# Optimization experiments

Hardware: AMD Instinct MI355X
Metric: run time of the kernel (lower is better)

Reference implementation:

```python
import jax, jax.numpy as jnp
import numpy as np

B, N, M, E, H = 8, 256, 512, 1024, 32
D = E // H
SCALING = D ** -0.5
BIG_DIST = 1e6


def setup_inputs() -> dict:
    key = jax.random.key(0)
    ks = jax.random.split(key, 12)
    w = lambda k: jax.random.normal(k, (E, E), jnp.float32) * 0.02
    return {
        "x": jax.random.normal(ks[0], (N, B, E), jnp.float32),
        "pos": jax.random.normal(ks[1], (B, N, 3), jnp.float32) * 3.0,
        "expand_pos": jax.random.normal(ks[2], (B, M, 3), jnp.float32) * 3.0,
        "attn_bias": jax.random.normal(ks[3], (B, H, N, N + M), jnp.float32) * 0.1,
        "padding_mask": jnp.zeros((B, N), bool),
        "expand_mask": jnp.zeros((B, M), bool),
        "outcell_index": jax.random.randint(ks[4], (B, M), 0, N),
        "Wq": w(ks[5]), "Wk": w(ks[6]), "Wv": w(ks[7]),
        "Wve": w(ks[8]), "Wo": w(ks[9]), "Woe": w(ks[10]),
    }


def reference(x, pos, expand_pos, attn_bias, padding_mask, expand_mask,
              outcell_index, Wq, Wk, Wv, Wve, Wo, Woe):
    xb = jnp.swapaxes(x, 0, 1)              # [B, N, E]
    b, n, e = xb.shape

    all_pos = jnp.concatenate([pos, expand_pos], axis=1)   # [B, EXT, 3]
    delta = pos[:, :, None, :] - all_pos[:, None, :, :]     # [B, N, EXT, 3]
    full_mask = jnp.concatenate([padding_mask, expand_mask], axis=-1)  # [B, EXT]

    dist = jnp.linalg.norm(delta, axis=-1)                  # [B, N, EXT]
    dist = jnp.where(padding_mask[:, :, None], BIG_DIST, dist)
    dist = jnp.where(full_mask[:, None, :], BIG_DIST, dist)
    delta = delta / (dist[..., None] + 1.0)

    q = (xb @ Wq.T) * SCALING
    k = xb @ Wk.T
    v = xb @ Wv.T
    ve = xb @ Wve.T

    gather = lambda t: jnp.take_along_axis(t, outcell_index[..., None], axis=1)
    k = jnp.concatenate([k, gather(k)], axis=1)             # [B, EXT, E]
    v = jnp.concatenate([v, gather(v)], axis=1)
    ve = jnp.concatenate([ve, gather(ve)], axis=1)
    ext = k.shape[1]

    qh = q.reshape(b, n, H, D).transpose(0, 2, 1, 3)        # [B, H, N, D]
    kh = k.reshape(b, ext, H, D).transpose(0, 2, 1, 3)
    vh = v.reshape(b, ext, H, D).transpose(0, 2, 1, 3)
    veh = ve.reshape(b, ext, H, D).transpose(0, 2, 1, 3)

    attn = jnp.einsum('bhnd,bhmd->bhnm', qh, kh) + attn_bias
    neg = jnp.finfo(jnp.float32).min
    attn = jnp.where(full_mask[:, None, None, :], neg, attn)
    attn = jnp.where(padding_mask[:, None, :, None], neg, attn)
    probs = jax.nn.softmax(attn.astype(jnp.float32), axis=-1).astype(attn.dtype)

    delta = jnp.where(padding_mask[:, :, None, None], 0.0, delta)

    # equivariant vector output: (probs ⊗ delta) contracted with v
    vec = jnp.einsum('bhnm,bnmc,bhmd->bnchd', probs, delta, vh)  # [B,N,3,H,D]
    vec_out = vec.reshape(b, n, 3, e) @ Wo.T

    xo = jnp.einsum('bhnm,bhmd->bnhd', probs, veh).reshape(b, n, e) @ Woe.T
    return (xo, vec_out)
```

## Files before the change

### kernel.cpp

```cpp
#include <hip/hip_runtime.h>


typedef unsigned short u16;
typedef unsigned int u32;
typedef short short8 __attribute__((ext_vector_type(8)));
typedef float float4v __attribute__((ext_vector_type(4)));

#define SCALING 0.17677669529663687f
#define LOG2E 1.4426950408889634f

__device__ __forceinline__ u16 f2b(float f) {
  union { float f; u32 u; } v; v.f = f;
  return (u16)((v.u + 0x7FFFu + ((v.u >> 16) & 1u)) >> 16);
}
__device__ __forceinline__ float b2f(short s) {
  union { u32 u; float f; } v; v.u = ((u32)(u16)s) << 16;
  return v.f;
}
__device__ __forceinline__ float4v mfma16(short8 a, short8 b, float4v c) {
  return __builtin_amdgcn_mfma_f32_16x16x32_bf16(a, b, c, 0, 0, 0);
}
__device__ __forceinline__ void gll16(const void* g, void* l) {
  __builtin_amdgcn_global_load_lds((const __attribute__((address_space(1))) void*)g,
                                   (__attribute__((address_space(3))) void*)l, 16, 0, 0);
}

__global__ __launch_bounds__(256) void convert_kernel(
    const float* __restrict__ x, const float* __restrict__ Wq,
    const float* __restrict__ Wk, const float* __restrict__ Wv,
    const float* __restrict__ Wve, const float* __restrict__ Wo,
    const float* __restrict__ Woe, u16* __restrict__ xb,
    u16* __restrict__ Wcat, u16* __restrict__ Woe_b, u16* __restrict__ Wo_b) {
  const int idx = blockIdx.x * 256 + threadIdx.x;
  const int stride = gridDim.x * 256;
  for (int i = idx; i < 2048 * 1024; i += stride) {
    const int row = i >> 10, e = i & 1023;
    const int b = row >> 8, n = row & 255;
    xb[i] = f2b(x[((size_t)n * 8 + b) * 1024 + e]);
  }
  for (int i = idx; i < 1024 * 1024; i += stride) {
    Wcat[i] = f2b(Wq[i]);
    Wcat[1048576 + i] = f2b(Wk[i]);
    Wcat[2097152 + i] = f2b(Wv[i]);
    Wcat[3145728 + i] = f2b(Wve[i]);
    Woe_b[i] = f2b(Woe[i]);
    Wo_b[i] = f2b(Wo[i]);
  }
}

__global__ __launch_bounds__(256) void gemm_bt(
    const u16* __restrict__ A, const u16* __restrict__ W_lo,
    const u16* __restrict__ W_hi, int split_row, float* __restrict__ C,
    int Ndim, int Kdim) {
  __shared__ __align__(16) u16 sA[128 * 32];
  __shared__ __align__(16) u16 sB[128 * 32];
  const int tid = threadIdx.x, wave = tid >> 6, lane = tid & 63;
  const int quad = lane >> 4, l15 = lane & 15;
  const int row0 = blockIdx.y * 128, col0 = blockIdx.x * 128;
  const u16* W = (row0 < split_row) ? W_lo : W_hi;
  const int wr = (wave >> 1) * 64, wc = (wave & 1) * 64;
  const int sr = lane >> 2, sc = lane & 3;
  float4v acc[4][4] = {};
  const u16* gA = A + (size_t)row0 * Kdim;
  const u16* gW = W + (size_t)col0 * Kdim;
  for (int k0 = 0; k0 < Kdim; k0 += 32) {
    __syncthreads();
#pragma unroll
    for (int i = 0; i < 2; ++i) {
      const int r = wave * 32 + i * 16 + sr;
      gll16(gA + (size_t)r * Kdim + k0 + sc * 8, (char*)sA + (wave * 32 + i * 16) * 64);
      gll16(gW + (size_t)r * Kdim + k0 + sc * 8, (char*)sB + (wave * 32 + i * 16) * 64);
    }
    __syncthreads();
    short8 af[4], bf[4];
#pragma unroll
    for (int t = 0; t < 4; ++t) {
      af[t] = *(const short8*)(sA + (wr + t * 16 + l15) * 32 + quad * 8);
      bf[t] = *(const short8*)(sB + (wc + t * 16 + l15) * 32 + quad * 8);
    }
#pragma unroll
    for (int tm = 0; tm < 4; ++tm)
#pragma unroll
      for (int tn = 0; tn < 4; ++tn)
        acc[tm][tn] = mfma16(af[tm], bf[tn], acc[tm][tn]);
  }
#pragma unroll
  for (int tm = 0; tm < 4; ++tm)
#pragma unroll
    for (int tn = 0; tn < 4; ++tn)
#pragma unroll
      for (int r = 0; r < 4; ++r) {
        const int row = row0 + wr + tm * 16 + quad * 4 + r;
        const int col = col0 + wc + tn * 16 + l15;
        C[(size_t)row * Ndim + col] = acc[tm][tn][r];
      }
}

__global__ __launch_bounds__(256) void shuffle_kernel(
    const float* __restrict__ proj, const int* __restrict__ outcell,
    u16* __restrict__ qrow, u16* __restrict__ kext,
    u16* __restrict__ vTx, u16* __restrict__ veTx) {
  __shared__ float lds[32 * 129];
  const int mt = blockIdx.x, h = blockIdx.y, b = blockIdx.z;
  const int tid = threadIdx.x;
  const int bh = b * 32 + h;
#pragma unroll 4
  for (int i = 0; i < 16; ++i) {
    const int idx = tid + 256 * i;
    const int ml = idx >> 5, d = idx & 31;
    const int m = mt * 128 + ml;
    const int src = (m < 256) ? m : outcell[b * 512 + m - 256];
    const size_t prow = ((size_t)b * 256 + src) * 4096;
    kext[((size_t)bh * 768 + m) * 32 + d] = f2b(proj[prow + 1024 + h * 32 + d]);
    if (m < 256)
      qrow[((size_t)bh * 256 + m) * 32 + d] = f2b(proj[prow + h * 32 + d] * SCALING);
  }
  for (int part = 0; part < 2; ++part) {
    const size_t cbase = (part == 0) ? 2048 : 3072;
    u16* dst = (part == 0) ? vTx : veTx;
    __syncthreads();
#pragma unroll 4
    for (int i = 0; i < 16; ++i) {
      const int idx = tid + 256 * i;
      const int ml = idx >> 5, d = idx & 31;
      const int m = mt * 128 + ml;
      const int src = (m < 256) ? m : outcell[b * 512 + m - 256];
      lds[d * 129 + ml] = proj[((size_t)b * 256 + src) * 4096 + cbase + h * 32 + d];
    }
    __syncthreads();
#pragma unroll 4
    for (int i = 0; i < 16; ++i) {
      const int idx = tid + 256 * i;
      const int d = idx >> 7, m2 = idx & 127;
      dst[((size_t)bh * 32 + d) * 768 + mt * 128 + m2] = f2b(lds[d * 129 + m2]);
    }
  }
}

__global__ __launch_bounds__(256) void fused_attn(
    const u16* __restrict__ qrow, const u16* __restrict__ kext,
    const u16* __restrict__ vTx, const u16* __restrict__ veTx,
    const float* __restrict__ bias, const float* __restrict__ pos,
    const float* __restrict__ epos, u16* __restrict__ xo_acc,
    u16* __restrict__ vec_acc) {
  __shared__ __align__(16) u16 sQ[64 * 32];
  __shared__ __align__(16) u16 sK[32 * 32];
  __shared__ __align__(16) u16 sV[32 * 32];
  __shared__ __align__(16) u16 sVe[32 * 32];
  __shared__ __align__(16) float sBias[64 * 32];
  __shared__ __align__(16) u16 sPT[4 * 16 * 40];
  __shared__ __align__(16) float sAP[768 * 3];
  const int nt = blockIdx.x, bh = blockIdx.y, b = bh >> 5, h = bh & 31;
  const int n0 = nt * 64;
  const int tid = threadIdx.x, w = tid >> 6, lane = tid & 63;
  const int quad = lane >> 4, l15 = lane & 15;
  gll16(qrow + ((size_t)bh * 256 + n0 + w * 16 + (lane >> 2)) * 32 + (lane & 3) * 8,
        (char*)sQ + w * 1024);
  const float* gp = pos + (size_t)b * 768;
  const float* ge = epos + (size_t)b * 1536;
  for (int i = w; i < 9; i += 4) {
    const float* src = (i < 3) ? (gp + i * 256) : (ge + (i - 3) * 256);
    gll16(src + lane * 4, (char*)sAP + i * 1024);
  }
  __syncthreads();
  const int nl = n0 + w * 16 + l15;
  const float px = sAP[nl * 3], py = sAP[nl * 3 + 1], pz = sAP[nl * 3 + 2];
  const short8 qf = *(const short8*)(sQ + (w * 16 + l15) * 32 + quad * 8);
  float4v acc[4][2] = {};
  float rowsum[4] = {0.f, 0.f, 0.f, 0.f};
  const u16* gK = kext + (size_t)bh * (768 * 32);
  const u16* gV = vTx + (size_t)bh * (32 * 768);
  const u16* gVe = veTx + (size_t)bh * (32 * 768);
  const float* gB = bias + ((size_t)bh * 256 + n0) * 768;
  u16* const pt = sPT + w * 640;
  for (int k0 = 0; k0 < 768; k0 += 32) {
    __syncthreads();
    if (w == 0) {
      gll16(gK + (size_t)(k0 + (lane >> 2)) * 32 + (lane & 3) * 8, (char*)sK);
      gll16(gK + (size_t)(k0 + 16 + (lane >> 2)) * 32 + (lane & 3) * 8, (char*)sK + 1024);
    } else if (w == 1) {
      gll16(gV + (size_t)(lane >> 2) * 768 + k0 + (lane & 3) * 8, (char*)sV);
      gll16(gV + (size_t)(16 + (lane >> 2)) * 768 + k0 + (lane & 3) * 8, (char*)sV + 1024);
    } else if (w == 2) {
      gll16(gVe + (size_t)(lane >> 2) * 768 + k0 + (lane & 3) * 8, (char*)sVe);
      gll16(gVe + (size_t)(16 + (lane >> 2)) * 768 + k0 + (lane & 3) * 8, (char*)sVe + 1024);
    }
    gll16(gB + (size_t)(w * 16 + (lane >> 3)) * 768 + k0 + (lane & 7) * 4,
          (char*)sBias + w * 2048);
    gll16(gB + (size_t)(w * 16 + 8 + (lane >> 3)) * 768 + k0 + (lane & 7) * 4,
          (char*)sBias + w * 2048 + 1024);
    __syncthreads();
    const short8 kf0 = *(const short8*)(sK + l15 * 32 + quad * 8);
    const short8 kf1 = *(const short8*)(sK + (16 + l15) * 32 + quad * 8);
    float4v z = {0.f, 0.f, 0.f, 0.f};
    const float4v s0 = mfma16(qf, kf0, z);
    const float4v s1 = mfma16(qf, kf1, z);
#pragma unroll
    for (int r = 0; r < 4; ++r) {
      const int row = quad * 4 + r;
      const float p0 = exp2f((s0[r] + sBias[(w * 16 + row) * 32 + l15]) * LOG2E);
      const float p1 = exp2f((s1[r] + sBias[(w * 16 + row) * 32 + 16 + l15]) * LOG2E);
      rowsum[r] += p0 + p1;
      pt[row * 40 + l15] = f2b(p0);
      pt[row * 40 + 16 + l15] = f2b(p1);
    }
    const short8 pf = *(const short8*)(pt + l15 * 40 + quad * 8);
    short8 bfe[2], bfv[2];
#pragma unroll
    for (int dt = 0; dt < 2; ++dt) {
      bfe[dt] = *(const short8*)(sVe + (dt * 16 + l15) * 32 + quad * 8);
      bfv[dt] = *(const short8*)(sV + (dt * 16 + l15) * 32 + quad * 8);
    }
    acc[0][0] = mfma16(pf, bfe[0], acc[0][0]);
    acc[0][1] = mfma16(pf, bfe[1], acc[0][1]);
    short8 pd0, pd1, pd2;
#pragma unroll
    for (int j = 0; j < 8; ++j) {
      const int m = k0 + quad * 8 + j;
      const float p = b2f(pf[j]);
      const float dx = px - sAP[m * 3];
      const float dy = py - sAP[m * 3 + 1];
      const float dz = pz - sAP[m * 3 + 2];
      const float dist = __builtin_amdgcn_sqrtf(dx * dx + dy * dy + dz * dz);
      const float pr = p * __builtin_amdgcn_rcpf(1.0f + dist);
      pd0[j] = (short)f2b(pr * dx);
      pd1[j] = (short)f2b(pr * dy);
      pd2[j] = (short)f2b(pr * dz);
    }
#pragma unroll
    for (int dt = 0; dt < 2; ++dt) {
      acc[1][dt] = mfma16(pd0, bfv[dt], acc[1][dt]);
      acc[2][dt] = mfma16(pd1, bfv[dt], acc[2][dt]);
      acc[3][dt] = mfma16(pd2, bfv[dt], acc[3][dt]);
    }
  }
  float li[4];
#pragma unroll
  for (int r = 0; r < 4; ++r) {
    float s = rowsum[r];
#pragma unroll
    for (int msk = 1; msk < 16; msk <<= 1) s += __shfl_xor(s, msk, 64);
    li[r] = __builtin_amdgcn_rcpf(s);
  }
#pragma unroll
  for (int t = 0; t < 4; ++t)
#pragma unroll
    for (int dt = 0; dt < 2; ++dt)
#pragma unroll
      for (int r = 0; r < 4; ++r) {
        const int row = n0 + w * 16 + quad * 4 + r;
        const int col = dt * 16 + l15;
        const float v = acc[t][dt][r] * li[r];
        if (t == 0)
          xo_acc[((size_t)b * 256 + row) * 1024 + h * 32 + col] = f2b(v);
        else
          vec_acc[(((size_t)b * 256 + row) * 3 + (t - 1)) * 1024 + h * 32 + col] = f2b(v);
      }
}

static constexpr size_t OFF_XB = 0;
static constexpr size_t OFF_WCAT = OFF_XB + 4194304;
static constexpr size_t OFF_WOEB = OFF_WCAT + 8388608;
static constexpr size_t OFF_WOB = OFF_WOEB + 2097152;
static constexpr size_t OFF_PROJ = OFF_WOB + 2097152;
static constexpr size_t OFF_QROW = OFF_PROJ + 33554432;
static constexpr size_t OFF_KEXT = OFF_QROW + 4194304;
static constexpr size_t OFF_VTX = OFF_KEXT + 12582912;
static constexpr size_t OFF_VETX = OFF_VTX + 12582912;
static constexpr size_t OFF_XOACC = OFF_VETX + 12582912;
static constexpr size_t OFF_VECACC = OFF_XOACC + 4194304;

extern "C" void kernel_launch(void* const* d_in, const int* in_sizes, int n_in,
                              void* d_out, int out_size, void* d_ws, size_t ws_size,
                              hipStream_t stream) {
  const float* x = (const float*)d_in[0];
  const float* pos = (const float*)d_in[1];
  const float* epos = (const float*)d_in[2];
  const float* bias = (const float*)d_in[3];
  const int* outcell = (const int*)d_in[6];
  const float* Wq = (const float*)d_in[7];
  const float* Wk = (const float*)d_in[8];
  const float* Wv = (const float*)d_in[9];
  const float* Wve = (const float*)d_in[10];
  const float* Wo = (const float*)d_in[11];
  const float* Woe = (const float*)d_in[12];
  char* ws = (char*)d_ws;
  u16* xb = (u16*)(ws + OFF_XB);
  u16* Wcat = (u16*)(ws + OFF_WCAT);
  u16* Woe_b = (u16*)(ws + OFF_WOEB);
  u16* Wo_b = (u16*)(ws + OFF_WOB);
  float* proj = (float*)(ws + OFF_PROJ);
  u16* qrow = (u16*)(ws + OFF_QROW);
  u16* kext = (u16*)(ws + OFF_KEXT);
  u16* vTx = (u16*)(ws + OFF_VTX);
  u16* veTx = (u16*)(ws + OFF_VETX);
  u16* xo_acc = (u16*)(ws + OFF_XOACC);
  u16* vec_acc = (u16*)(ws + OFF_VECACC);
  float* out = (float*)d_out;

  convert_kernel<<<1024, 256, 0, stream>>>(x, Wq, Wk, Wv, Wve, Wo, Woe,
                                           xb, Wcat, Woe_b, Wo_b);
  gemm_bt<<<dim3(32, 16), 256, 0, stream>>>(xb, Wcat, Wcat, 1 << 30, proj, 4096, 1024);
  shuffle_kernel<<<dim3(6, 32, 8), 256, 0, stream>>>(proj, outcell, qrow, kext, vTx, veTx);
  fused_attn<<<dim3(4, 256), 256, 0, stream>>>(qrow, kext, vTx, veTx, bias, pos, epos,
                                               xo_acc, vec_acc);
  gemm_bt<<<dim3(8, 64), 256, 0, stream>>>(xo_acc, Woe_b, Wo_b, 2048, out, 1024, 1024);
}
```

Baseline: 467.8 us.

## Precompute weighted deltas, bf16 projections, fold scale into Wq, double-buffer attention

```diff
diff --git a/kernel.cpp b/kernel.cpp
--- a/kernel.cpp
+++ b/kernel.cpp
@@ -5,9 +5,12 @@
 typedef unsigned int u32;
 typedef short short8 __attribute__((ext_vector_type(8)));
 typedef float float4v __attribute__((ext_vector_type(4)));
+typedef u32 u32x4 __attribute__((ext_vector_type(4)));
 
 #define SCALING 0.17677669529663687f
 #define LOG2E 1.4426950408889634f
+#define QSCALE (SCALING * LOG2E)
+#define WDPLANE 1572864
 
 __device__ __forceinline__ u16 f2b(float f) {
   union { float f; u32 u; } v; v.f = f;
@@ -16,6 +19,23 @@
 __device__ __forceinline__ float b2f(short s) {
   union { u32 u; float f; } v; v.u = ((u32)(u16)s) << 16;
   return v.f;
+}
+__device__ __forceinline__ u16 rb16(float f) {
+  union { float f; u32 u; } v; v.f = f;
+  return (u16)((v.u + 0x8000u) >> 16);
+}
+__device__ __forceinline__ float bitf(u32 u) {
+  union { u32 u; float f; } v; v.u = u; return v.f;
+}
+__device__ __forceinline__ u32 biti(float f) {
+  union { float f; u32 u; } v; v.f = f; return v.u;
+}
+__device__ __forceinline__ u32 pdpair(u32 pw, u32 ww) {
+  const float pa = bitf(pw << 16), pb = bitf(pw & 0xFFFF0000u);
+  const float wa = bitf(ww << 16), wb = bitf(ww & 0xFFFF0000u);
+  const u32 ra = biti(pa * wa) + 0x8000u;
+  const u32 rb = biti(pb * wb) + 0x8000u;
+  return __builtin_amdgcn_perm(rb, ra, 0x07060302);
 }
 __device__ __forceinline__ float4v mfma16(short8 a, short8 b, float4v c) {
   return __builtin_amdgcn_mfma_f32_16x16x32_bf16(a, b, c, 0, 0, 0);
@@ -29,8 +49,10 @@
     const float* __restrict__ x, const float* __restrict__ Wq,
     const float* __restrict__ Wk, const float* __restrict__ Wv,
     const float* __restrict__ Wve, const float* __restrict__ Wo,
-    const float* __restrict__ Woe, u16* __restrict__ xb,
-    u16* __restrict__ Wcat, u16* __restrict__ Woe_b, u16* __restrict__ Wo_b) {
+    const float* __restrict__ Woe, const float* __restrict__ pos,
+    const float* __restrict__ epos, u16* __restrict__ xb,
+    u16* __restrict__ Wcat, u16* __restrict__ Woe_b, u16* __restrict__ Wo_b,
+    u16* __restrict__ wd) {
   const int idx = blockIdx.x * 256 + threadIdx.x;
   const int stride = gridDim.x * 256;
   for (int i = idx; i < 2048 * 1024; i += stride) {
@@ -39,19 +61,34 @@
     xb[i] = f2b(x[((size_t)n * 8 + b) * 1024 + e]);
   }
   for (int i = idx; i < 1024 * 1024; i += stride) {
-    Wcat[i] = f2b(Wq[i]);
+    Wcat[i] = f2b(Wq[i] * QSCALE);
     Wcat[1048576 + i] = f2b(Wk[i]);
     Wcat[2097152 + i] = f2b(Wv[i]);
     Wcat[3145728 + i] = f2b(Wve[i]);
     Woe_b[i] = f2b(Woe[i]);
     Wo_b[i] = f2b(Wo[i]);
   }
+  for (int i = idx; i < 8 * 256 * 768; i += stride) {
+    const int m = i % 768, t = i / 768;
+    const int n = t & 255, b = t >> 8;
+    const float qx = pos[((size_t)b * 256 + n) * 3];
+    const float qy = pos[((size_t)b * 256 + n) * 3 + 1];
+    const float qz = pos[((size_t)b * 256 + n) * 3 + 2];
+    const float* ap = (m < 256) ? (pos + ((size_t)b * 256 + m) * 3)
+                                : (epos + ((size_t)b * 512 + m - 256) * 3);
+    const float dx = qx - ap[0], dy = qy - ap[1], dz = qz - ap[2];
+    const float dist = __builtin_amdgcn_sqrtf(dx * dx + dy * dy + dz * dz);
+    const float w = __builtin_amdgcn_rcpf(1.0f + dist);
+    wd[i] = f2b(dx * w);
+    wd[WDPLANE + i] = f2b(dy * w);
+    wd[2 * WDPLANE + i] = f2b(dz * w);
+  }
 }
 
 __global__ __launch_bounds__(256) void gemm_bt(
     const u16* __restrict__ A, const u16* __restrict__ W_lo,
-    const u16* __restrict__ W_hi, int split_row, float* __restrict__ C,
-    int Ndim, int Kdim) {
+    const u16* __restrict__ W_hi, int split_row, void* __restrict__ Cout,
+    int Ndim, int Kdim, int bf16_out) {
   __shared__ __align__(16) u16 sA[128 * 32];
   __shared__ __align__(16) u16 sB[128 * 32];
   const int tid = threadIdx.x, wave = tid >> 6, lane = tid & 63;
@@ -92,15 +129,17 @@
       for (int r = 0; r < 4; ++r) {
         const int row = row0 + wr + tm * 16 + quad * 4 + r;
         const int col = col0 + wc + tn * 16 + l15;
-        C[(size_t)row * Ndim + col] = acc[tm][tn][r];
+        if (bf16_out)
+          ((u16*)Cout)[(size_t)row * Ndim + col] = f2b(acc[tm][tn][r]);
+        else
+          ((float*)Cout)[(size_t)row * Ndim + col] = acc[tm][tn][r];
       }
 }
 
 __global__ __launch_bounds__(256) void shuffle_kernel(
-    const float* __restrict__ proj, const int* __restrict__ outcell,
-    u16* __restrict__ qrow, u16* __restrict__ kext,
-    u16* __restrict__ vTx, u16* __restrict__ veTx) {
-  __shared__ float lds[32 * 129];
+    const u16* __restrict__ proj, const int* __restrict__ outcell,
+    u16* __restrict__ kext, u16* __restrict__ vTx, u16* __restrict__ veTx) {
+  __shared__ u16 lds[32 * 129];
   const int mt = blockIdx.x, h = blockIdx.y, b = blockIdx.z;
   const int tid = threadIdx.x;
   const int bh = b * 32 + h;
@@ -110,10 +149,8 @@
     const int ml = idx >> 5, d = idx & 31;
     const int m = mt * 128 + ml;
     const int src = (m < 256) ? m : outcell[b * 512 + m - 256];
-    const size_t prow = ((size_t)b * 256 + src) * 4096;
-    kext[((size_t)bh * 768 + m) * 32 + d] = f2b(proj[prow + 1024 + h * 32 + d]);
-    if (m < 256)
-      qrow[((size_t)bh * 256 + m) * 32 + d] = f2b(proj[prow + h * 32 + d] * SCALING);
+    kext[((size_t)bh * 768 + m) * 32 + d] =
+        proj[((size_t)b * 256 + src) * 4096 + 1024 + h * 32 + d];
   }
   for (int part = 0; part < 2; ++part) {
     const size_t cbase = (part == 0) ? 2048 : 3072;
@@ -132,107 +169,102 @@
     for (int i = 0; i < 16; ++i) {
       const int idx = tid + 256 * i;
       const int d = idx >> 7, m2 = idx & 127;
-      dst[((size_t)bh * 32 + d) * 768 + mt * 128 + m2] = f2b(lds[d * 129 + m2]);
-    }
-  }
-}
-
-__global__ __launch_bounds__(256) void fused_attn(
-    const u16* __restrict__ qrow, const u16* __restrict__ kext,
+      dst[((size_t)bh * 32 + d) * 768 + mt * 128 + m2] = lds[d * 129 + m2];
+    }
+  }
+}
+
+__global__ __launch_bounds__(256, 4) void fused_attn(
+    const u16* __restrict__ proj, const u16* __restrict__ kext,
     const u16* __restrict__ vTx, const u16* __restrict__ veTx,
-    const float* __restrict__ bias, const float* __restrict__ pos,
-    const float* __restrict__ epos, u16* __restrict__ xo_acc,
-    u16* __restrict__ vec_acc) {
-  __shared__ __align__(16) u16 sQ[64 * 32];
-  __shared__ __align__(16) u16 sK[32 * 32];
-  __shared__ __align__(16) u16 sV[32 * 32];
-  __shared__ __align__(16) u16 sVe[32 * 32];
-  __shared__ __align__(16) float sBias[64 * 32];
+    const float* __restrict__ bias, const u16* __restrict__ wd,
+    u16* __restrict__ xo_acc, u16* __restrict__ vec_acc) {
+  __shared__ __align__(16) u16 sK[2][32 * 32];
+  __shared__ __align__(16) u16 sV[2][32 * 32];
+  __shared__ __align__(16) u16 sVe[2][32 * 32];
+  __shared__ __align__(16) float sBias[2][64 * 32];
   __shared__ __align__(16) u16 sPT[4 * 16 * 40];
-  __shared__ __align__(16) float sAP[768 * 3];
   const int nt = blockIdx.x, bh = blockIdx.y, b = bh >> 5, h = bh & 31;
   const int n0 = nt * 64;
   const int tid = threadIdx.x, w = tid >> 6, lane = tid & 63;
   const int quad = lane >> 4, l15 = lane & 15;
-  gll16(qrow + ((size_t)bh * 256 + n0 + w * 16 + (lane >> 2)) * 32 + (lane & 3) * 8,
-        (char*)sQ + w * 1024);
-  const float* gp = pos + (size_t)b * 768;
-  const float* ge = epos + (size_t)b * 1536;
-  for (int i = w; i < 9; i += 4) {
-    const float* src = (i < 3) ? (gp + i * 256) : (ge + (i - 3) * 256);
-    gll16(src + lane * 4, (char*)sAP + i * 1024);
-  }
-  __syncthreads();
-  const int nl = n0 + w * 16 + l15;
-  const float px = sAP[nl * 3], py = sAP[nl * 3 + 1], pz = sAP[nl * 3 + 2];
-  const short8 qf = *(const short8*)(sQ + (w * 16 + l15) * 32 + quad * 8);
-  float4v acc[4][2] = {};
-  float rowsum[4] = {0.f, 0.f, 0.f, 0.f};
+  const short8 qf = *(const short8*)(
+      proj + ((size_t)b * 256 + n0 + w * 16 + l15) * 4096 + h * 32 + quad * 8);
   const u16* gK = kext + (size_t)bh * (768 * 32);
   const u16* gV = vTx + (size_t)bh * (32 * 768);
   const u16* gVe = veTx + (size_t)bh * (32 * 768);
   const float* gB = bias + ((size_t)bh * 256 + n0) * 768;
+  const u16* wdp = wd + ((size_t)b * 256 + n0 + w * 16 + l15) * 768;
   u16* const pt = sPT + w * 640;
-  for (int k0 = 0; k0 < 768; k0 += 32) {
-    __syncthreads();
+
+  auto stage = [&](int t, int buf) {
+    const int kk = t * 32;
     if (w == 0) {
-      gll16(gK + (size_t)(k0 + (lane >> 2)) * 32 + (lane & 3) * 8, (char*)sK);
-      gll16(gK + (size_t)(k0 + 16 + (lane >> 2)) * 32 + (lane & 3) * 8, (char*)sK + 1024);
+      gll16(gK + (size_t)(kk + (lane >> 2)) * 32 + (lane & 3) * 8, (char*)sK[buf]);
+      gll16(gK + (size_t)(kk + 16 + (lane >> 2)) * 32 + (lane & 3) * 8, (char*)sK[buf] + 1024);
     } else if (w == 1) {
-      gll16(gV + (size_t)(lane >> 2) * 768 + k0 + (lane & 3) * 8, (char*)sV);
-      gll16(gV + (size_t)(16 + (lane >> 2)) * 768 + k0 + (lane & 3) * 8, (char*)sV + 1024);
+      gll16(gV + (size_t)(lane >> 2) * 768 + kk + (lane & 3) * 8, (char*)sV[buf]);
+      gll16(gV + (size_t)(16 + (lane >> 2)) * 768 + kk + (lane & 3) * 8, (char*)sV[buf] + 1024);
     } else if (w == 2) {
-      gll16(gVe + (size_t)(lane >> 2) * 768 + k0 + (lane & 3) * 8, (char*)sVe);
-      gll16(gVe + (size_t)(16 + (lane >> 2)) * 768 + k0 + (lane & 3) * 8, (char*)sVe + 1024);
-    }
-    gll16(gB + (size_t)(w * 16 + (lane >> 3)) * 768 + k0 + (lane & 7) * 4,
-          (char*)sBias + w * 2048);
-    gll16(gB + (size_t)(w * 16 + 8 + (lane >> 3)) * 768 + k0 + (lane & 7) * 4,
-          (char*)sBias + w * 2048 + 1024);
-    __syncthreads();
-    const short8 kf0 = *(const short8*)(sK + l15 * 32 + quad * 8);
-    const short8 kf1 = *(const short8*)(sK + (16 + l15) * 32 + quad * 8);
+      gll16(gVe + (size_t)(lane >> 2) * 768 + kk + (lane & 3) * 8, (char*)sVe[buf]);
+      gll16(gVe + (size_t)(16 + (lane >> 2)) * 768 + kk + (lane & 3) * 8, (char*)sVe[buf] + 1024);
+    }
+    gll16(gB + (size_t)(w * 16 + (lane >> 3)) * 768 + kk + (lane & 7) * 4,
+          (char*)sBias[buf] + w * 2048);
+    gll16(gB + (size_t)(w * 16 + 8 + (lane >> 3)) * 768 + kk + (lane & 7) * 4,
+          (char*)sBias[buf] + w * 2048 + 1024);
+  };
+
+  float4v acc[4][2] = {};
+  float rowsum[4] = {0.f, 0.f, 0.f, 0.f};
+  stage(0, 0);
+  for (int t = 0; t < 24; ++t) {
+    const int k0 = t * 32, buf = t & 1;
+    __syncthreads();
+    if (t < 23) stage(t + 1, buf ^ 1);
+    const short8 w8x = *(const short8*)(wdp + k0 + quad * 8);
+    const short8 w8y = *(const short8*)(wdp + WDPLANE + k0 + quad * 8);
+    const short8 w8z = *(const short8*)(wdp + 2 * WDPLANE + k0 + quad * 8);
+    const short8 kf0 = *(const short8*)(sK[buf] + l15 * 32 + quad * 8);
+    const short8 kf1 = *(const short8*)(sK[buf] + (16 + l15) * 32 + quad * 8);
     float4v z = {0.f, 0.f, 0.f, 0.f};
     const float4v s0 = mfma16(qf, kf0, z);
     const float4v s1 = mfma16(qf, kf1, z);
 #pragma unroll
     for (int r = 0; r < 4; ++r) {
-      const int row = quad * 4 + r;
-      const float p0 = exp2f((s0[r] + sBias[(w * 16 + row) * 32 + l15]) * LOG2E);
-      const float p1 = exp2f((s1[r] + sBias[(w * 16 + row) * 32 + 16 + l15]) * LOG2E);
+      const int row = w * 16 + quad * 4 + r;
+      const float p0 = __builtin_amdgcn_exp2f(
+          __builtin_fmaf(sBias[buf][row * 32 + l15], LOG2E, s0[r]));
+      const float p1 = __builtin_amdgcn_exp2f(
+          __builtin_fmaf(sBias[buf][row * 32 + 16 + l15], LOG2E, s1[r]));
       rowsum[r] += p0 + p1;
-      pt[row * 40 + l15] = f2b(p0);
-      pt[row * 40 + 16 + l15] = f2b(p1);
+      pt[(quad * 4 + r) * 40 + l15] = rb16(p0);
+      pt[(quad * 4 + r) * 40 + 16 + l15] = rb16(p1);
     }
     const short8 pf = *(const short8*)(pt + l15 * 40 + quad * 8);
-    short8 bfe[2], bfv[2];
-#pragma unroll
-    for (int dt = 0; dt < 2; ++dt) {
-      bfe[dt] = *(const short8*)(sVe + (dt * 16 + l15) * 32 + quad * 8);
-      bfv[dt] = *(const short8*)(sV + (dt * 16 + l15) * 32 + quad * 8);
-    }
-    acc[0][0] = mfma16(pf, bfe[0], acc[0][0]);
-    acc[0][1] = mfma16(pf, bfe[1], acc[0][1]);
-    short8 pd0, pd1, pd2;
-#pragma unroll
-    for (int j = 0; j < 8; ++j) {
-      const int m = k0 + quad * 8 + j;
-      const float p = b2f(pf[j]);
-      const float dx = px - sAP[m * 3];
-      const float dy = py - sAP[m * 3 + 1];
-      const float dz = pz - sAP[m * 3 + 2];
-      const float dist = __builtin_amdgcn_sqrtf(dx * dx + dy * dy + dz * dz);
-      const float pr = p * __builtin_amdgcn_rcpf(1.0f + dist);
-      pd0[j] = (short)f2b(pr * dx);
-      pd1[j] = (short)f2b(pr * dy);
-      pd2[j] = (short)f2b(pr * dz);
-    }
-#pragma unroll
-    for (int dt = 0; dt < 2; ++dt) {
-      acc[1][dt] = mfma16(pd0, bfv[dt], acc[1][dt]);
-      acc[2][dt] = mfma16(pd1, bfv[dt], acc[2][dt]);
-      acc[3][dt] = mfma16(pd2, bfv[dt], acc[3][dt]);
-    }
+    const short8 bfe0 = *(const short8*)(sVe[buf] + l15 * 32 + quad * 8);
+    const short8 bfe1 = *(const short8*)(sVe[buf] + (16 + l15) * 32 + quad * 8);
+    const short8 bfv0 = *(const short8*)(sV[buf] + l15 * 32 + quad * 8);
+    const short8 bfv1 = *(const short8*)(sV[buf] + (16 + l15) * 32 + quad * 8);
+    acc[0][0] = mfma16(pf, bfe0, acc[0][0]);
+    acc[0][1] = mfma16(pf, bfe1, acc[0][1]);
+    u32x4 a0, a1, a2;
+#pragma unroll
+    for (int jp = 0; jp < 4; ++jp) {
+      const u32 pw = ((const u32*)&pf)[jp];
+      a0[jp] = pdpair(pw, ((const u32*)&w8x)[jp]);
+      a1[jp] = pdpair(pw, ((const u32*)&w8y)[jp]);
+      a2[jp] = pdpair(pw, ((const u32*)&w8z)[jp]);
+    }
+    const short8 pd0 = *(const short8*)&a0;
+    const short8 pd1 = *(const short8*)&a1;
+    const short8 pd2 = *(const short8*)&a2;
+    acc[1][0] = mfma16(pd0, bfv0, acc[1][0]);
+    acc[1][1] = mfma16(pd0, bfv1, acc[1][1]);
+    acc[2][0] = mfma16(pd1, bfv0, acc[2][0]);
+    acc[2][1] = mfma16(pd1, bfv1, acc[2][1]);
+    acc[3][0] = mfma16(pd2, bfv0, acc[3][0]);
+    acc[3][1] = mfma16(pd2, bfv1, acc[3][1]);
   }
   float li[4];
 #pragma unroll
@@ -263,11 +295,11 @@
 static constexpr size_t OFF_WOEB = OFF_WCAT + 8388608;
 static constexpr size_t OFF_WOB = OFF_WOEB + 2097152;
 static constexpr size_t OFF_PROJ = OFF_WOB + 2097152;
-static constexpr size_t OFF_QROW = OFF_PROJ + 33554432;
-static constexpr size_t OFF_KEXT = OFF_QROW + 4194304;
+static constexpr size_t OFF_KEXT = OFF_PROJ + 16777216;
 static constexpr size_t OFF_VTX = OFF_KEXT + 12582912;
 static constexpr size_t OFF_VETX = OFF_VTX + 12582912;
-static constexpr size_t OFF_XOACC = OFF_VETX + 12582912;
+static constexpr size_t OFF_WD = OFF_VETX + 12582912;
+static constexpr size_t OFF_XOACC = OFF_WD + 9437184;
 static constexpr size_t OFF_VECACC = OFF_XOACC + 4194304;
 
 extern "C" void kernel_launch(void* const* d_in, const int* in_sizes, int n_in,
@@ -289,20 +321,20 @@
   u16* Wcat = (u16*)(ws + OFF_WCAT);
   u16* Woe_b = (u16*)(ws + OFF_WOEB);
   u16* Wo_b = (u16*)(ws + OFF_WOB);
-  float* proj = (float*)(ws + OFF_PROJ);
-  u16* qrow = (u16*)(ws + OFF_QROW);
+  u16* proj = (u16*)(ws + OFF_PROJ);
   u16* kext = (u16*)(ws + OFF_KEXT);
   u16* vTx = (u16*)(ws + OFF_VTX);
   u16* veTx = (u16*)(ws + OFF_VETX);
+  u16* wdw = (u16*)(ws + OFF_WD);
   u16* xo_acc = (u16*)(ws + OFF_XOACC);
   u16* vec_acc = (u16*)(ws + OFF_VECACC);
   float* out = (float*)d_out;
 
-  convert_kernel<<<1024, 256, 0, stream>>>(x, Wq, Wk, Wv, Wve, Wo, Woe,
-                                           xb, Wcat, Woe_b, Wo_b);
-  gemm_bt<<<dim3(32, 16), 256, 0, stream>>>(xb, Wcat, Wcat, 1 << 30, proj, 4096, 1024);
-  shuffle_kernel<<<dim3(6, 32, 8), 256, 0, stream>>>(proj, outcell, qrow, kext, vTx, veTx);
-  fused_attn<<<dim3(4, 256), 256, 0, stream>>>(qrow, kext, vTx, veTx, bias, pos, epos,
+  convert_kernel<<<1024, 256, 0, stream>>>(x, Wq, Wk, Wv, Wve, Wo, Woe, pos, epos,
+                                           xb, Wcat, Woe_b, Wo_b, wdw);
+  gemm_bt<<<dim3(32, 16), 256, 0, stream>>>(xb, Wcat, Wcat, 1 << 30, proj, 4096, 1024, 1);
+  shuffle_kernel<<<dim3(6, 32, 8), 256, 0, stream>>>(proj, outcell, kext, vTx, veTx);
+  fused_attn<<<dim3(4, 256), 256, 0, stream>>>(proj, kext, vTx, veTx, bias, wdw,
                                                xo_acc, vec_acc);
-  gemm_bt<<<dim3(8, 64), 256, 0, stream>>>(xo_acc, Woe_b, Wo_b, 2048, out, 1024, 1024);
-}
+  gemm_bt<<<dim3(8, 64), 256, 0, stream>>>(xo_acc, Woe_b, Wo_b, 2048, out, 1024, 1024, 0);
+}
```

Measured after the change: 479.2 us. +2.4%, slower.
